# Optimization experiments

Hardware: AMD Instinct MI355X
Metric: run time of the kernel (lower is better)

The kernel has to match this reference:

```python
import jax, jax.numpy as jnp
import numpy as np

B = 8
A = 1614
TOPN = 6
IOU_THR = 0.25
PAD = 224
OUT = 224

def _make_anchors():
    # 6 anchor shapes on the 14x14 map, 6 on 7x7, 9 on 4x4 -> 1614 total,
    # ordered anchor-type-major then row-major spatial to match the [C,H,W] flatten
    # of the tidy conv outputs (as generate_default_anchor_maps does in NTS-Net).
    specs = [
        (14, 32.0, [(48, 48), (64, 48), (48, 64), (80, 80), (96, 64), (64, 96)]),
        (7, 64.0, [(96, 96), (128, 96), (96, 128), (160, 160), (192, 128), (128, 192)]),
        (4, 112.0, [(192, 192), (256, 192), (192, 256), (288, 288), (320, 256), (256, 320), (352, 352), (384, 320), (320, 384)]),
    ]
    blocks = []
    for fm, stride, sizes in specs:
        c = (np.arange(fm) + 0.5) * stride
        cy, cx = np.meshgrid(c, c, indexing='ij')
        for (h, w) in sizes:
            blocks.append(np.stack([cy - h / 2, cx - w / 2, cy + h / 2, cx + w / 2], -1).reshape(-1, 4))
    a = (np.concatenate(blocks, 0) + PAD).astype(np.int64)  # mimic (edge_anchors+224).astype(int)
    return a.astype(np.float32)  # [1614,4] (y0,x0,y1,x1) in padded-image coords

def _conv(x, w, b, stride, pad):
    y = jax.lax.conv_general_dilated(x, w, (stride, stride), [(pad, pad), (pad, pad)],
                                     dimension_numbers=('NCHW', 'OIHW', 'NCHW'))
    return y + b[None, :, None, None]

def _rpn_scores(rpn, wd1, bd1, wd2, bd2, wd3, bd3, wt1, bt1, wt2, bt2, wt3, bt3):
    b = rpn.shape[0]
    d1 = jax.nn.relu(_conv(rpn, wd1, bd1, 1, 1))   # [B,128,14,14]
    d2 = jax.nn.relu(_conv(d1, wd2, bd2, 2, 1))    # [B,128,7,7]
    d3 = jax.nn.relu(_conv(d2, wd3, bd3, 2, 1))    # [B,128,4,4]
    t1 = _conv(d1, wt1, bt1, 1, 0).reshape(b, -1)  # [B,1176]
    t2 = _conv(d2, wt2, bt2, 1, 0).reshape(b, -1)  # [B,294]
    t3 = _conv(d3, wt3, bt3, 1, 0).reshape(b, -1)  # [B,144]
    return jnp.concatenate([t1, t2, t3], axis=1)   # [B,1614]

def _nms_keep(boxes, scores):
    # Greedy NMS over all A anchors; returns keep mask in ORIGINAL anchor order.
    order = jnp.argsort(-scores)
    b = boxes[order]
    y0, x0, y1, x1 = b[:, 0], b[:, 1], b[:, 2], b[:, 3]
    area = (y1 - y0) * (x1 - x0)
    ih = jnp.clip(jnp.minimum(y1[:, None], y1[None, :]) - jnp.maximum(y0[:, None], y0[None, :]), 0)
    iw = jnp.clip(jnp.minimum(x1[:, None], x1[None, :]) - jnp.maximum(x0[:, None], x0[None, :]), 0)
    inter = ih * iw
    iou = inter / (area[:, None] + area[None, :] - inter)
    idx = jnp.arange(A)
    def body(i, supp):
        row = (iou[i] > IOU_THR) & (idx > i)
        return jnp.where(supp[i], supp, supp | row)
    supp = jax.lax.fori_loop(0, A, body, jnp.zeros((A,), bool))
    return jnp.zeros((A,), bool).at[order].set(~supp)

def _crop_resize(img, box):
    # img [3,Hp,Wp]; box int32 (x0,y0,x1,y1).
    # Equivalent to F.interpolate(img[:, y0:y1, x0:x1], (224,224), 'bilinear', align_corners=True)
    x0, y0, x1, y1 = box[0], box[1], box[2], box[3]
    t = jnp.arange(OUT, dtype=jnp.float32) / (OUT - 1)
    sy = y0.astype(jnp.float32) + t * (y1 - 1 - y0).astype(jnp.float32)
    sx = x0.astype(jnp.float32) + t * (x1 - 1 - x0).astype(jnp.float32)
    y0i = jnp.floor(sy).astype(jnp.int32); x0i = jnp.floor(sx).astype(jnp.int32)
    y1i = jnp.minimum(y0i + 1, y1 - 1);    x1i = jnp.minimum(x0i + 1, x1 - 1)
    wy = (sy - y0i.astype(jnp.float32))[None, :, None]
    wx = (sx - x0i.astype(jnp.float32))[None, None, :]
    g = lambda yi, xi: img[:, yi][:, :, xi]  # gather rows then cols -> [3,224,224]
    top = (1 - wx) * g(y0i, x0i) + wx * g(y0i, x1i)
    bot = (1 - wx) * g(y1i, x0i) + wx * g(y1i, x1i)
    return (1 - wy) * top + wy * bot

def setup_inputs():
    key = jax.random.key(0)
    ks = jax.random.split(key, 16)
    n = jax.random.normal
    return {
        'x': n(ks[0], (B, 3, 448, 448), jnp.float32),
        'rpn_feature': n(ks[1], (B, 2048, 14, 14), jnp.float32),
        'anchors': jnp.asarray(_make_anchors()),
        'wd1': 0.02 * n(ks[2], (128, 2048, 3, 3), jnp.float32), 'bd1': 0.01 * n(ks[3], (128,), jnp.float32),
        'wd2': 0.05 * n(ks[4], (128, 128, 3, 3), jnp.float32),  'bd2': 0.01 * n(ks[5], (128,), jnp.float32),
        'wd3': 0.05 * n(ks[6], (128, 128, 3, 3), jnp.float32),  'bd3': 0.01 * n(ks[7], (128,), jnp.float32),
        'wt1': 0.1 * n(ks[8], (6, 128, 1, 1), jnp.float32),     'bt1': 0.01 * n(ks[9], (6,), jnp.float32),
        'wt2': 0.1 * n(ks[10], (6, 128, 1, 1), jnp.float32),    'bt2': 0.01 * n(ks[11], (6,), jnp.float32),
        'wt3': 0.1 * n(ks[12], (9, 128, 1, 1), jnp.float32),    'bt3': 0.01 * n(ks[13], (9,), jnp.float32),
    }

def reference(x, rpn_feature, anchors, wd1, bd1, wd2, bd2, wd3, bd3, wt1, bt1, wt2, bt2, wt3, bt3):
    scores = _rpn_scores(rpn_feature, wd1, bd1, wd2, bd2, wd3, bd3, wt1, bt1, wt2, bt2, wt3, bt3)
    keep = jax.vmap(lambda s: _nms_keep(anchors, s))(scores)           # [B,A] bool
    masked = jnp.where(keep, scores, -jnp.inf)
    top_prob, top_idx = jax.lax.top_k(masked, TOPN)                    # [B,6]
    tb = anchors[top_idx]                                              # [B,6,4] (y0,x0,y1,x1)
    coords = jnp.stack([tb[..., 1], tb[..., 0], tb[..., 3], tb[..., 2]], -1)  # (x0,y0,x1,y1)
    x_pad = jnp.pad(x, ((0, 0), (0, 0), (PAD, PAD), (PAD, PAD)))       # [B,3,896,896]
    bint = coords.astype(jnp.int32)
    part_imgs = jax.vmap(lambda img, bs: jax.vmap(lambda bb: _crop_resize(img, bb))(bs))(x_pad, bint)  # [B,6,3,224,224]
    return part_imgs, coords, top_prob, top_idx
```

## Files before the change

### kernel.cpp

```cpp
#include <hip/hip_runtime.h>
#include <hip/hip_bf16.h>
#include <math.h>
#include <stdint.h>


#define OFF_COORDS 7225344
#define OFF_PROB   7225536
#define OFF_IDX    7225584
#define NA 1614
#define K1TOT 18432

typedef __attribute__((ext_vector_type(8)))  short  short8;
typedef __attribute__((ext_vector_type(16))) float  floatx16;

__device__ inline void split_bf16(float v, unsigned short& h, unsigned short& l)
{
    __hip_bfloat16 hb = __float2bfloat16(v);
    float hv = __bfloat162float(hb);
    __hip_bfloat16 lb = __float2bfloat16(v - hv);
    h = *reinterpret_cast<unsigned short*>(&hb);
    l = *reinterpret_cast<unsigned short*>(&lb);
}

__global__ __launch_bounds__(256) void k_prep(const float* __restrict__ rpn,
                                              const float* __restrict__ w1,
                                              const float* __restrict__ w2,
                                              const float* __restrict__ w3,
                                              unsigned short* __restrict__ ah,
                                              unsigned short* __restrict__ al,
                                              unsigned short* __restrict__ b1h,
                                              unsigned short* __restrict__ b1l,
                                              unsigned short* __restrict__ b2h,
                                              unsigned short* __restrict__ b2l,
                                              unsigned short* __restrict__ b3h,
                                              unsigned short* __restrict__ b3l)
{
    __shared__ float tileA[64][65];
    __shared__ float tileB[9][260];
    const int bid = blockIdx.x;
    const int t   = threadIdx.x;

    if (bid < 1024) {
        const int cib  = (bid & 31) * 64;
        const int posb = ((bid >> 5) & 3) * 64;
        const int b    = bid >> 7;
#pragma unroll
        for (int it = 0; it < 16; ++it) {
            int idx  = it * 256 + t;
            int cil  = idx >> 6;
            int posl = idx & 63;
            int pos  = posb + posl;
            int py = pos >> 4, px = pos & 15;
            int y = py - 1, x = px - 1;
            float v = 0.0f;
            if ((unsigned)y < 14u && (unsigned)x < 14u)
                v = rpn[((size_t)(b * 2048 + cib + cil) * 14 + y) * 14 + x];
            tileA[cil][posl] = v;
        }
        __syncthreads();
#pragma unroll
        for (int it = 0; it < 16; ++it) {
            int idx  = it * 256 + t;
            int posl = idx >> 6;
            int cil  = idx & 63;
            float v = tileA[cil][posl];
            unsigned short h, l;
            split_bf16(v, h, l);
            size_t o = (size_t)(b * 256 + posb + posl) * 2048 + cib + cil;
            ah[o] = h; al[o] = l;
        }
    } else if (bid < 2048) {
        const int lb  = bid - 1024;
        const int ci0 = (lb & 7) * 256;
        const int co  = lb >> 3;
        const float* wc = w1 + (size_t)co * K1TOT + (size_t)ci0 * 9;
#pragma unroll
        for (int it = 0; it < 9; ++it) {
            int i = it * 256 + t;
            float v = wc[i];
            tileB[i % 9][i / 9] = v;
        }
        __syncthreads();
#pragma unroll
        for (int tap = 0; tap < 9; ++tap) {
            float v = tileB[tap][t];
            unsigned short h, l;
            split_bf16(v, h, l);
            size_t o = (size_t)co * K1TOT + (size_t)tap * 2048 + ci0 + t;
            b1h[o] = h; b1l[o] = l;
        }
    } else {
        const int lb  = bid - 2048;
        const int tap = lb % 9;
        const int co  = lb / 9;
        const int z   = t >> 7;
        const int ci  = t & 127;
        const float* w = z ? w3 : w2;
        unsigned short* bh = z ? b3h : b2h;
        unsigned short* bl = z ? b3l : b2l;
        float v = w[((size_t)co * 128 + ci) * 9 + tap];
        unsigned short h, l;
        split_bf16(v, h, l);
        size_t o = (size_t)co * 1152 + tap * 128 + ci;
        bh[o] = h; bl[o] = l;
    }
}

template<int POSN, int OW, int STR, int CIN, int MTOT>
__global__ __launch_bounds__(128) void k_conv64(const short* __restrict__ ah,
                                                const short* __restrict__ al,
                                                const short* __restrict__ bh,
                                                const short* __restrict__ bl,
                                                float* __restrict__ partial,
                                                int chunk)
{
    constexpr int KTOT = CIN * 9;
    __shared__ short AsH[64][40];
    __shared__ short AsL[64][40];
    __shared__ short BsH[128][40];
    __shared__ short BsL[128][40];

    const int t     = threadIdx.x;
    const int lane  = t & 63;
    const int w     = t >> 6;
    const int wn    = w * 64;
    const int lm    = lane & 31;
    const int half  = lane >> 5;
    const int mbase = blockIdx.x * 64;
    const int kc    = blockIdx.y;
    const int k0    = kc * chunk;
    const int k1    = (k0 + chunk < KTOT) ? (k0 + chunk) : KTOT;

    const int akc = (t & 3) * 8;
    int arow[2], apos[2]; bool aval[2];
#pragma unroll
    for (int i = 0; i < 2; ++i) {
        int slot = i * 128 + t;
        int row  = slot >> 2;
        int m    = mbase + row;
        arow[i] = row;
        aval[i] = (m < MTOT);
        int mm = aval[i] ? m : 0;
        int b  = mm / POSN;
        int p  = mm - b * POSN;
        int y  = p / OW;
        int x  = p - y * OW;
        apos[i] = b * 256 + y * STR * 16 + x * STR;
    }

    floatx16 acc[2][2];
#pragma unroll
    for (int mf = 0; mf < 2; ++mf)
#pragma unroll
        for (int nf = 0; nf < 2; ++nf)
#pragma unroll
            for (int r = 0; r < 16; ++r) acc[mf][nf][r] = 0.0f;

    const short8 zero8 = {0, 0, 0, 0, 0, 0, 0, 0};

    for (int ks = k0; ks < k1; ks += 32) {
        const int tap = ks / CIN;
        const int ci0 = ks - tap * CIN;
        const int dy  = tap / 3, dx = tap - dy * 3;
#pragma unroll
        for (int i = 0; i < 2; ++i) {
            short8 vh = zero8, vl = zero8;
            if (aval[i]) {
                size_t g = (size_t)(apos[i] + dy * 16 + dx) * CIN + ci0 + akc;
                vh = *(const short8*)(ah + g);
                vl = *(const short8*)(al + g);
            }
            *(short8*)&AsH[arow[i]][akc] = vh;
            *(short8*)&AsL[arow[i]][akc] = vl;
        }
#pragma unroll
        for (int j = 0; j < 4; ++j) {
            int n = ((j * 128 + t) >> 2);
            size_t g = (size_t)n * KTOT + ks + akc;
            *(short8*)&BsH[n][akc] = *(const short8*)(bh + g);
            *(short8*)&BsL[n][akc] = *(const short8*)(bl + g);
        }
        __syncthreads();
#pragma unroll
        for (int kst = 0; kst < 2; ++kst) {
            const int koff = kst * 16 + half * 8;
            short8 a_h[2], a_l[2], b_h[2], b_l[2];
#pragma unroll
            for (int mf = 0; mf < 2; ++mf) {
                a_h[mf] = *(const short8*)&AsH[mf * 32 + lm][koff];
                a_l[mf] = *(const short8*)&AsL[mf * 32 + lm][koff];
            }
#pragma unroll
            for (int nf = 0; nf < 2; ++nf) {
                b_h[nf] = *(const short8*)&BsH[wn + nf * 32 + lm][koff];
                b_l[nf] = *(const short8*)&BsL[wn + nf * 32 + lm][koff];
            }
#pragma unroll
            for (int mf = 0; mf < 2; ++mf)
#pragma unroll
                for (int nf = 0; nf < 2; ++nf) {
                    acc[mf][nf] = __builtin_amdgcn_mfma_f32_32x32x16_bf16(
                        a_h[mf], b_h[nf], acc[mf][nf], 0, 0, 0);
                    acc[mf][nf] = __builtin_amdgcn_mfma_f32_32x32x16_bf16(
                        a_h[mf], b_l[nf], acc[mf][nf], 0, 0, 0);
                    acc[mf][nf] = __builtin_amdgcn_mfma_f32_32x32x16_bf16(
                        a_l[mf], b_h[nf], acc[mf][nf], 0, 0, 0);
                }
        }
        __syncthreads();
    }

    float* P = partial + (size_t)kc * MTOT * 128;
#pragma unroll
    for (int mf = 0; mf < 2; ++mf)
#pragma unroll
        for (int nf = 0; nf < 2; ++nf)
#pragma unroll
            for (int r = 0; r < 16; ++r) {
                int row = (r & 3) + 8 * (r >> 2) + 4 * half;
                int m = mbase + mf * 32 + row;
                int n = wn + nf * 32 + lm;
                if (m < MTOT) P[(size_t)m * 128 + n] = acc[mf][nf][r];
            }
}

template<int POSN, int OWV>
__global__ __launch_bounds__(256) void k_reduce_pad(const float* __restrict__ partial,
                                                    const float* __restrict__ bias,
                                                    float* __restrict__ dn,
                                                    __hip_bfloat16* __restrict__ ph,
                                                    __hip_bfloat16* __restrict__ pl,
                                                    int S)
{
    constexpr int MTOT = 8 * POSN;
    int idx = blockIdx.x * 256 + threadIdx.x;
    int b   = idx >> 13;
    int pos = (idx >> 5) & 255;
    int c4  = idx & 31;
    int y = (pos >> 4) - 1;
    int x = (pos & 15) - 1;
    if ((unsigned)y < (unsigned)OWV && (unsigned)x < (unsigned)OWV) {
        int m = b * POSN + y * OWV + x;
        float4 s = ((const float4*)bias)[c4];
        for (int k = 0; k < S; ++k) {
            float4 p = ((const float4*)(partial + (size_t)k * MTOT * 128 + (size_t)m * 128))[c4];
            s.x += p.x; s.y += p.y; s.z += p.z; s.w += p.w;
        }
        s.x = fmaxf(s.x, 0.0f); s.y = fmaxf(s.y, 0.0f);
        s.z = fmaxf(s.z, 0.0f); s.w = fmaxf(s.w, 0.0f);
        ((float4*)dn)[(size_t)m * 32 + c4] = s;
        ushort4 h, l;
        split_bf16(s.x, h.x, l.x);
        split_bf16(s.y, h.y, l.y);
        split_bf16(s.z, h.z, l.z);
        split_bf16(s.w, h.w, l.w);
        ((ushort4*)ph)[idx] = h;
        ((ushort4*)pl)[idx] = l;
    } else {
        ushort4 z = {0, 0, 0, 0};
        ((ushort4*)ph)[idx] = z;
        ((ushort4*)pl)[idx] = z;
    }
}

__global__ __launch_bounds__(256) void k_reduce3(const float* __restrict__ partial,
                                                 const float* __restrict__ bias,
                                                 float* __restrict__ dn, int S)
{
    int idx = blockIdx.x * 256 + threadIdx.x;
    int c4  = idx & 31;
    float4 s = ((const float4*)bias)[c4];
    for (int k = 0; k < S; ++k) {
        float4 p = ((const float4*)(partial + (size_t)k * 128 * 128))[idx];
        s.x += p.x; s.y += p.y; s.z += p.z; s.w += p.w;
    }
    s.x = fmaxf(s.x, 0.0f); s.y = fmaxf(s.y, 0.0f);
    s.z = fmaxf(s.z, 0.0f); s.w = fmaxf(s.w, 0.0f);
    ((float4*)dn)[idx] = s;
}

__global__ __launch_bounds__(512) void k_headnms(const float* __restrict__ d1n,
                                                 const float* __restrict__ d2n,
                                                 const float* __restrict__ d3n,
                                                 const float* __restrict__ w1, const float* __restrict__ b1,
                                                 const float* __restrict__ w2, const float* __restrict__ b2,
                                                 const float* __restrict__ w3, const float* __restrict__ b3,
                                                 const float* __restrict__ anchors,
                                                 float* __restrict__ out,
                                                 int* __restrict__ boxes)
{
    __shared__ float ms[NA];
    __shared__ float ay0[NA], ax0[NA], ay1[NA], ax1[NA];
    __shared__ unsigned char picked[NA];
    __shared__ float wsm[21 * 128];
    __shared__ float bsm[21];
    __shared__ float rv[8]; __shared__ int ri[8];
    __shared__ float win[5];
    const int b = blockIdx.x;
    const int t = threadIdx.x;

    for (int i = t; i < 21 * 128; i += 512)
        wsm[i] = (i < 768) ? w1[i] : (i < 1536) ? w2[i - 768] : w3[i - 1536];
    if (t < 21) bsm[t] = (t < 6) ? b1[t] : (t < 12) ? b2[t - 6] : b3[t - 12];
    for (int i = t; i < NA; i += 512) {
        float4 an = ((const float4*)anchors)[i];
        ay0[i] = an.x; ax0[i] = an.y; ay1[i] = an.z; ax1[i] = an.w;
        picked[i] = 0;
    }
    __syncthreads();

    for (int e = t; e < NA; e += 512) {
        const float* d; int wrow;
        if (e < 1176) {
            int c = e / 196, p = e - c * 196;
            d = d1n + (size_t)(b * 196 + p) * 128; wrow = c;
        } else if (e < 1470) {
            int e2 = e - 1176; int c = e2 / 49, p = e2 - c * 49;
            d = d2n + (size_t)(b * 49 + p) * 128; wrow = 6 + c;
        } else {
            int e2 = e - 1470; int c = e2 / 16, p = e2 - c * 16;
            d = d3n + (size_t)(b * 16 + p) * 128; wrow = 12 + c;
        }
        float s = bsm[wrow];
        const float4* wv4 = (const float4*)&wsm[wrow * 128];
#pragma unroll
        for (int i = 0; i < 32; ++i) {
            float4 dv = ((const float4*)d)[i];
            float4 wv = wv4[i];
            s = fmaf(dv.x, wv.x, s);
            s = fmaf(dv.y, wv.y, s);
            s = fmaf(dv.z, wv.z, s);
            s = fmaf(dv.w, wv.w, s);
        }
        ms[e] = s;
    }
    __syncthreads();

    for (int r = 0; r < 6; ++r) {
        float bv = -INFINITY; int bi = NA;
        for (int i = t; i < NA; i += 512) {
            if (!picked[i]) {
                float v = ms[i];
                if (v > bv || (v == bv && i < bi)) { bv = v; bi = i; }
            }
        }
#pragma unroll
        for (int off = 32; off > 0; off >>= 1) {
            float v2 = __shfl_down(bv, off);
            int   i2 = __shfl_down(bi, off);
            if (v2 > bv || (v2 == bv && i2 < bi)) { bv = v2; bi = i2; }
        }
        if ((t & 63) == 0) { rv[t >> 6] = bv; ri[t >> 6] = bi; }
        __syncthreads();
        if (t == 0) {
            bv = rv[0]; bi = ri[0];
            for (int wv = 1; wv < 8; ++wv)
                if (rv[wv] > bv || (rv[wv] == bv && ri[wv] < bi)) { bv = rv[wv]; bi = ri[wv]; }
            picked[bi] = 1;
            win[0] = ay0[bi]; win[1] = ax0[bi]; win[2] = ay1[bi]; win[3] = ax1[bi]; win[4] = bv;
            int o = b * 6 + r;
            out[OFF_COORDS + o * 4 + 0] = ax0[bi];
            out[OFF_COORDS + o * 4 + 1] = ay0[bi];
            out[OFF_COORDS + o * 4 + 2] = ax1[bi];
            out[OFF_COORDS + o * 4 + 3] = ay1[bi];
            out[OFF_PROB + o] = bv;
            out[OFF_IDX  + o] = (float)bi;
            boxes[o * 4 + 0] = (int)ax0[bi];
            boxes[o * 4 + 1] = (int)ay0[bi];
            boxes[o * 4 + 2] = (int)ax1[bi];
            boxes[o * 4 + 3] = (int)ay1[bi];
        }
        __syncthreads();
        float by0 = win[0], bx0 = win[1], by1 = win[2], bx1 = win[3];
        float barea = (by1 - by0) * (bx1 - bx0);
        for (int i = t; i < NA; i += 512) {
            if (picked[i]) continue;
            float ih = fmaxf(fminf(by1, ay1[i]) - fmaxf(by0, ay0[i]), 0.0f);
            float iw = fmaxf(fminf(bx1, ax1[i]) - fmaxf(bx0, ax0[i]), 0.0f);
            float inter = ih * iw;
            float area  = (ay1[i] - ay0[i]) * (ax1[i] - ax0[i]);
            float iou = inter / (barea + area - inter);
            if (iou > 0.25f) ms[i] = -INFINITY;
        }
        __syncthreads();
    }
}

__global__ __launch_bounds__(256) void k_crop(const float* __restrict__ x,
                                              const int* __restrict__ boxes,
                                              float* __restrict__ out)
{
    int idx = blockIdx.x * 256 + threadIdx.x;
    int i   = idx % 224;
    int j   = (idx / 224) % 224;
    int rem = idx / 50176;
    int c   = rem % 3;
    int br  = rem / 3;
    int b   = br / 6;
    int4 bx = ((const int4*)boxes)[br];
    float tj = (float)j / 223.0f;
    float sy = (float)bx.y + tj * (float)(bx.w - 1 - bx.y);
    int y0i = (int)floorf(sy);
    int y1i = min(y0i + 1, bx.w - 1);
    float wy = sy - (float)y0i;
    float ti = (float)i / 223.0f;
    float sx = (float)bx.x + ti * (float)(bx.z - 1 - bx.x);
    int x0i = (int)floorf(sx);
    int x1i = min(x0i + 1, bx.z - 1);
    float wx = sx - (float)x0i;
    const float* img = x + ((size_t)b * 3 + c) * 448 * 448;
    auto g = [&](int yy, int xx) -> float {
        yy -= 224; xx -= 224;
        if ((unsigned)yy >= 448u || (unsigned)xx >= 448u) return 0.0f;
        return img[(size_t)yy * 448 + xx];
    };
    float g00 = g(y0i, x0i), g01 = g(y0i, x1i);
    float g10 = g(y1i, x0i), g11 = g(y1i, x1i);
    float top = (1.0f - wx) * g00 + wx * g01;
    float bot = (1.0f - wx) * g10 + wx * g11;
    out[idx] = (1.0f - wy) * top + wy * bot;
}

extern "C" void kernel_launch(void* const* d_in, const int* in_sizes, int n_in,
                              void* d_out, int out_size, void* d_ws, size_t ws_size,
                              hipStream_t stream)
{
    (void)in_sizes; (void)n_in; (void)out_size;
    const float* x    = (const float*)d_in[0];
    const float* rpn  = (const float*)d_in[1];
    const float* anch = (const float*)d_in[2];
    const float* wd1  = (const float*)d_in[3];
    const float* bd1  = (const float*)d_in[4];
    const float* wd2  = (const float*)d_in[5];
    const float* bd2  = (const float*)d_in[6];
    const float* wd3  = (const float*)d_in[7];
    const float* bd3  = (const float*)d_in[8];
    const float* hw1  = (const float*)d_in[9];
    const float* hb1  = (const float*)d_in[10];
    const float* hw2  = (const float*)d_in[11];
    const float* hb2  = (const float*)d_in[12];
    const float* hw3  = (const float*)d_in[13];
    const float* hb3  = (const float*)d_in[14];
    float* out = (float*)d_out;

    char* ws = (char*)d_ws;
    size_t off = 0;
    auto alloc = [&](size_t bytes) -> void* {
        void* p = ws + off;
        off = (off + bytes + 255) & ~(size_t)255;
        return p;
    };
    unsigned short* ahb = (unsigned short*)alloc((size_t)8 * 256 * 2048 * 2);
    unsigned short* alb = (unsigned short*)alloc((size_t)8 * 256 * 2048 * 2);
    unsigned short* b1h = (unsigned short*)alloc((size_t)128 * K1TOT * 2);
    unsigned short* b1l = (unsigned short*)alloc((size_t)128 * K1TOT * 2);
    unsigned short* b2h = (unsigned short*)alloc((size_t)128 * 1152 * 2);
    unsigned short* b2l = (unsigned short*)alloc((size_t)128 * 1152 * 2);
    unsigned short* b3h = (unsigned short*)alloc((size_t)128 * 1152 * 2);
    unsigned short* b3l = (unsigned short*)alloc((size_t)128 * 1152 * 2);
    __hip_bfloat16* d1ph = (__hip_bfloat16*)alloc((size_t)8 * 256 * 128 * 2);
    __hip_bfloat16* d1pl = (__hip_bfloat16*)alloc((size_t)8 * 256 * 128 * 2);
    __hip_bfloat16* d2ph = (__hip_bfloat16*)alloc((size_t)8 * 256 * 128 * 2);
    __hip_bfloat16* d2pl = (__hip_bfloat16*)alloc((size_t)8 * 256 * 128 * 2);
    float* d1n  = (float*)alloc((size_t)8 * 196 * 128 * 4);
    float* d2n  = (float*)alloc((size_t)8 * 49 * 128 * 4);
    float* d3n  = (float*)alloc((size_t)8 * 16 * 128 * 4);
    int*  boxes = (int*)alloc((size_t)8 * 6 * 4 * 4);
    size_t avail = (ws_size > off) ? (ws_size - off) : 0;
    float* P = (float*)(ws + off);

    long long s1 = (long long)(avail / ((size_t)1568 * 128 * 4));
    if (s1 > 48) s1 = 48;
    if (s1 < 1)  s1 = 1;
    int S1 = (int)s1;
    int chunk1 = ((K1TOT + S1 * 32 - 1) / (S1 * 32)) * 32;

    long long s2 = (long long)(avail / ((size_t)392 * 128 * 4));
    if (s2 > 36) s2 = 36;
    if (s2 < 1)  s2 = 1;
    int S2 = (int)s2;
    int chunk2 = ((1152 + S2 * 32 - 1) / (S2 * 32)) * 32;

    long long s3 = (long long)(avail / ((size_t)128 * 128 * 4));
    if (s3 > 36) s3 = 36;
    if (s3 < 1)  s3 = 1;
    int S3 = (int)s3;
    int chunk3 = ((1152 + S3 * 32 - 1) / (S3 * 32)) * 32;

    k_prep<<<dim3(3200), 256, 0, stream>>>(rpn, wd1, wd2, wd3,
        ahb, alb, b1h, b1l, b2h, b2l, b3h, b3l);

    k_conv64<196, 14, 1, 2048, 1568><<<dim3(25, S1), 128, 0, stream>>>(
        (const short*)ahb, (const short*)alb, (const short*)b1h, (const short*)b1l, P, chunk1);
    k_reduce_pad<196, 14><<<dim3(256), 256, 0, stream>>>(P, bd1, d1n, d1ph, d1pl, S1);

    k_conv64<49, 7, 2, 128, 392><<<dim3(7, S2), 128, 0, stream>>>(
        (const short*)d1ph, (const short*)d1pl, (const short*)b2h, (const short*)b2l, P, chunk2);
    k_reduce_pad<49, 7><<<dim3(256), 256, 0, stream>>>(P, bd2, d2n, d2ph, d2pl, S2);

    k_conv64<16, 4, 2, 128, 128><<<dim3(2, S3), 128, 0, stream>>>(
        (const short*)d2ph, (const short*)d2pl, (const short*)b3h, (const short*)b3l, P, chunk3);
    k_reduce3<<<dim3(16), 256, 0, stream>>>(P, bd3, d3n, S3);

    k_headnms<<<dim3(8), 512, 0, stream>>>(d1n, d2n, d3n,
        hw1, hb1, hw2, hb2, hw3, hb3, anch, out, boxes);

    k_crop<<<dim3(28224), 256, 0, stream>>>(x, boxes, out);
}
```

Measured before the change: 276.6 us.

## Use 128x128 MFMA conv tile, split head scoring from NMS, vectorize crop

Adds a 256-thread conv kernel with a 128x128 output tile (2x2 waves, 2x2 MFMA fragments) for the large first conv. This raises reuse of each loaded B tile and halves the number of M blocks. The head 1x1 convs move out of the 8-block NMS kernel into a grid-wide kernel, so only the NMS/top-k runs per batch. The crop now writes four outputs per thread as a float4. The split-K counts for conv2 and conv3 are hardcoded to 36, which assumes the workspace is large enough.

```diff
diff --git a/kernel.cpp b/kernel.cpp
--- a/kernel.cpp
+++ b/kernel.cpp
@@ -107,6 +107,123 @@
 }
 
 template<int POSN, int OW, int STR, int CIN, int MTOT>
+__global__ __launch_bounds__(256) void k_conv_mfma(const short* __restrict__ ah,
+                                                   const short* __restrict__ al,
+                                                   const short* __restrict__ bh,
+                                                   const short* __restrict__ bl,
+                                                   float* __restrict__ partial,
+                                                   int chunk)
+{
+    constexpr int KTOT = CIN * 9;
+    __shared__ short AsH[128][40];
+    __shared__ short AsL[128][40];
+    __shared__ short BsH[128][40];
+    __shared__ short BsL[128][40];
+
+    const int t     = threadIdx.x;
+    const int lane  = t & 63;
+    const int w     = t >> 6;
+    const int wm    = (w & 1) * 64;
+    const int wn    = (w >> 1) * 64;
+    const int lm    = lane & 31;
+    const int half  = lane >> 5;
+    const int mbase = blockIdx.x * 128;
+    const int k0    = blockIdx.y * chunk;
+    const int k1    = (k0 + chunk < KTOT) ? (k0 + chunk) : KTOT;
+
+    int arow[2], apos[2]; bool aval[2];
+    const int akc = (t & 3) * 8;
+#pragma unroll
+    for (int i = 0; i < 2; ++i) {
+        int row = ((i * 256 + t) >> 2);
+        int m   = mbase + row;
+        arow[i] = row;
+        aval[i] = (m < MTOT);
+        int mm = aval[i] ? m : 0;
+        int b  = mm / POSN;
+        int p  = mm - b * POSN;
+        int y  = p / OW;
+        int x  = p - y * OW;
+        apos[i] = b * 256 + y * STR * 16 + x * STR;
+    }
+
+    floatx16 acc[2][2];
+#pragma unroll
+    for (int mf = 0; mf < 2; ++mf)
+#pragma unroll
+        for (int nf = 0; nf < 2; ++nf)
+#pragma unroll
+            for (int r = 0; r < 16; ++r) acc[mf][nf][r] = 0.0f;
+
+    const short8 zero8 = {0, 0, 0, 0, 0, 0, 0, 0};
+
+    for (int ks = k0; ks < k1; ks += 32) {
+        const int tap = ks / CIN;
+        const int ci0 = ks - tap * CIN;
+        const int dy  = tap / 3, dx = tap - dy * 3;
+#pragma unroll
+        for (int i = 0; i < 2; ++i) {
+            short8 vh = zero8, vl = zero8;
+            if (aval[i]) {
+                size_t g = (size_t)(apos[i] + dy * 16 + dx) * CIN + ci0 + akc;
+                vh = *(const short8*)(ah + g);
+                vl = *(const short8*)(al + g);
+            }
+            *(short8*)&AsH[arow[i]][akc] = vh;
+            *(short8*)&AsL[arow[i]][akc] = vl;
+        }
+#pragma unroll
+        for (int i = 0; i < 2; ++i) {
+            int n = ((i * 256 + t) >> 2);
+            size_t g = (size_t)n * KTOT + ks + akc;
+            *(short8*)&BsH[n][akc] = *(const short8*)(bh + g);
+            *(short8*)&BsL[n][akc] = *(const short8*)(bl + g);
+        }
+        __syncthreads();
+#pragma unroll
+        for (int kst = 0; kst < 2; ++kst) {
+            const int koff = kst * 16 + half * 8;
+            short8 a_h[2], a_l[2], b_h[2], b_l[2];
+#pragma unroll
+            for (int mf = 0; mf < 2; ++mf) {
+                a_h[mf] = *(const short8*)&AsH[wm + mf * 32 + lm][koff];
+                a_l[mf] = *(const short8*)&AsL[wm + mf * 32 + lm][koff];
+            }
+#pragma unroll
+            for (int nf = 0; nf < 2; ++nf) {
+                b_h[nf] = *(const short8*)&BsH[wn + nf * 32 + lm][koff];
+                b_l[nf] = *(const short8*)&BsL[wn + nf * 32 + lm][koff];
+            }
+#pragma unroll
+            for (int mf = 0; mf < 2; ++mf)
+#pragma unroll
+                for (int nf = 0; nf < 2; ++nf) {
+                    acc[mf][nf] = __builtin_amdgcn_mfma_f32_32x32x16_bf16(
+                        a_h[mf], b_h[nf], acc[mf][nf], 0, 0, 0);
+                    acc[mf][nf] = __builtin_amdgcn_mfma_f32_32x32x16_bf16(
+                        a_h[mf], b_l[nf], acc[mf][nf], 0, 0, 0);
+                    acc[mf][nf] = __builtin_amdgcn_mfma_f32_32x32x16_bf16(
+                        a_l[mf], b_h[nf], acc[mf][nf], 0, 0, 0);
+                }
+        }
+        __syncthreads();
+    }
+
+    float* P = partial + (size_t)blockIdx.y * MTOT * 128;
+#pragma unroll
+    for (int mf = 0; mf < 2; ++mf)
+#pragma unroll
+        for (int nf = 0; nf < 2; ++nf)
+#pragma unroll
+            for (int r = 0; r < 16; ++r) {
+                int row = (r & 3) + 8 * (r >> 2) + 4 * half;
+                int m = mbase + wm + mf * 32 + row;
+                int n = wn + nf * 32 + lm;
+                if (m < MTOT) P[(size_t)m * 128 + n] = acc[mf][nf][r];
+            }
+}
+
+template<int POSN, int OW, int STR, int CIN, int MTOT>
 __global__ __launch_bounds__(128) void k_conv64(const short* __restrict__ ah,
                                                 const short* __restrict__ al,
                                                 const short* __restrict__ bh,
@@ -279,66 +396,64 @@
     ((float4*)dn)[idx] = s;
 }
 
-__global__ __launch_bounds__(512) void k_headnms(const float* __restrict__ d1n,
-                                                 const float* __restrict__ d2n,
-                                                 const float* __restrict__ d3n,
-                                                 const float* __restrict__ w1, const float* __restrict__ b1,
-                                                 const float* __restrict__ w2, const float* __restrict__ b2,
-                                                 const float* __restrict__ w3, const float* __restrict__ b3,
-                                                 const float* __restrict__ anchors,
-                                                 float* __restrict__ out,
-                                                 int* __restrict__ boxes)
+__global__ __launch_bounds__(256) void k_heads(const float* __restrict__ d1n,
+                                               const float* __restrict__ d2n,
+                                               const float* __restrict__ d3n,
+                                               const float* __restrict__ w1, const float* __restrict__ b1,
+                                               const float* __restrict__ w2, const float* __restrict__ b2,
+                                               const float* __restrict__ w3, const float* __restrict__ b3,
+                                               float* __restrict__ scores)
+{
+    int idx = blockIdx.x * 256 + threadIdx.x;
+    if (idx >= 8 * NA) return;
+    int b = idx / NA;
+    int e = idx - b * NA;
+    const float* d; const float* w; float bias;
+    if (e < 1176) {
+        int c = e / 196, p = e - c * 196;
+        d = d1n + (size_t)(b * 196 + p) * 128; w = w1 + c * 128; bias = b1[c];
+    } else if (e < 1470) {
+        int e2 = e - 1176; int c = e2 / 49, p = e2 - c * 49;
+        d = d2n + (size_t)(b * 49 + p) * 128; w = w2 + c * 128; bias = b2[c];
+    } else {
+        int e2 = e - 1470; int c = e2 / 16, p = e2 - c * 16;
+        d = d3n + (size_t)(b * 16 + p) * 128; w = w3 + c * 128; bias = b3[c];
+    }
+    float s = bias;
+#pragma unroll
+    for (int i = 0; i < 32; ++i) {
+        float4 dv = ((const float4*)d)[i];
+        float4 wv = ((const float4*)w)[i];
+        s = fmaf(dv.x, wv.x, s);
+        s = fmaf(dv.y, wv.y, s);
+        s = fmaf(dv.z, wv.z, s);
+        s = fmaf(dv.w, wv.w, s);
+    }
+    scores[idx] = s;
+}
+
+__global__ __launch_bounds__(256) void k_nms_topk(const float* __restrict__ scores,
+                                                  const float* __restrict__ anchors,
+                                                  float* __restrict__ out,
+                                                  int* __restrict__ boxes)
 {
     __shared__ float ms[NA];
     __shared__ float ay0[NA], ax0[NA], ay1[NA], ax1[NA];
     __shared__ unsigned char picked[NA];
-    __shared__ float wsm[21 * 128];
-    __shared__ float bsm[21];
-    __shared__ float rv[8]; __shared__ int ri[8];
+    __shared__ float rv[4]; __shared__ int ri[4];
     __shared__ float win[5];
-    const int b = blockIdx.x;
-    const int t = threadIdx.x;
-
-    for (int i = t; i < 21 * 128; i += 512)
-        wsm[i] = (i < 768) ? w1[i] : (i < 1536) ? w2[i - 768] : w3[i - 1536];
-    if (t < 21) bsm[t] = (t < 6) ? b1[t] : (t < 12) ? b2[t - 6] : b3[t - 12];
-    for (int i = t; i < NA; i += 512) {
+    int b = blockIdx.x;
+    int t = threadIdx.x;
+    for (int i = t; i < NA; i += 256) {
+        ms[i] = scores[b * NA + i];
         float4 an = ((const float4*)anchors)[i];
         ay0[i] = an.x; ax0[i] = an.y; ay1[i] = an.z; ax1[i] = an.w;
         picked[i] = 0;
     }
     __syncthreads();
-
-    for (int e = t; e < NA; e += 512) {
-        const float* d; int wrow;
-        if (e < 1176) {
-            int c = e / 196, p = e - c * 196;
-            d = d1n + (size_t)(b * 196 + p) * 128; wrow = c;
-        } else if (e < 1470) {
-            int e2 = e - 1176; int c = e2 / 49, p = e2 - c * 49;
-            d = d2n + (size_t)(b * 49 + p) * 128; wrow = 6 + c;
-        } else {
-            int e2 = e - 1470; int c = e2 / 16, p = e2 - c * 16;
-            d = d3n + (size_t)(b * 16 + p) * 128; wrow = 12 + c;
-        }
-        float s = bsm[wrow];
-        const float4* wv4 = (const float4*)&wsm[wrow * 128];
-#pragma unroll
-        for (int i = 0; i < 32; ++i) {
-            float4 dv = ((const float4*)d)[i];
-            float4 wv = wv4[i];
-            s = fmaf(dv.x, wv.x, s);
-            s = fmaf(dv.y, wv.y, s);
-            s = fmaf(dv.z, wv.z, s);
-            s = fmaf(dv.w, wv.w, s);
-        }
-        ms[e] = s;
-    }
-    __syncthreads();
-
     for (int r = 0; r < 6; ++r) {
         float bv = -INFINITY; int bi = NA;
-        for (int i = t; i < NA; i += 512) {
+        for (int i = t; i < NA; i += 256) {
             if (!picked[i]) {
                 float v = ms[i];
                 if (v > bv || (v == bv && i < bi)) { bv = v; bi = i; }
@@ -354,7 +469,7 @@
         __syncthreads();
         if (t == 0) {
             bv = rv[0]; bi = ri[0];
-            for (int wv = 1; wv < 8; ++wv)
+            for (int wv = 1; wv < 4; ++wv)
                 if (rv[wv] > bv || (rv[wv] == bv && ri[wv] < bi)) { bv = rv[wv]; bi = ri[wv]; }
             picked[bi] = 1;
             win[0] = ay0[bi]; win[1] = ax0[bi]; win[2] = ay1[bi]; win[3] = ax1[bi]; win[4] = bv;
@@ -373,7 +488,7 @@
         __syncthreads();
         float by0 = win[0], bx0 = win[1], by1 = win[2], bx1 = win[3];
         float barea = (by1 - by0) * (bx1 - bx0);
-        for (int i = t; i < NA; i += 512) {
+        for (int i = t; i < NA; i += 256) {
             if (picked[i]) continue;
             float ih = fmaxf(fminf(by1, ay1[i]) - fmaxf(by0, ay0[i]), 0.0f);
             float iw = fmaxf(fminf(bx1, ax1[i]) - fmaxf(bx0, ax0[i]), 0.0f);
@@ -386,14 +501,14 @@
     }
 }
 
-__global__ __launch_bounds__(256) void k_crop(const float* __restrict__ x,
-                                              const int* __restrict__ boxes,
-                                              float* __restrict__ out)
+__global__ __launch_bounds__(256) void k_crop4(const float* __restrict__ x,
+                                               const int* __restrict__ boxes,
+                                               float* __restrict__ out)
 {
     int idx = blockIdx.x * 256 + threadIdx.x;
-    int i   = idx % 224;
-    int j   = (idx / 224) % 224;
-    int rem = idx / 50176;
+    int qi  = idx % 56;
+    int j   = (idx / 56) % 224;
+    int rem = idx / (56 * 224);
     int c   = rem % 3;
     int br  = rem / 3;
     int b   = br / 6;
@@ -403,22 +518,30 @@
     int y0i = (int)floorf(sy);
     int y1i = min(y0i + 1, bx.w - 1);
     float wy = sy - (float)y0i;
-    float ti = (float)i / 223.0f;
-    float sx = (float)bx.x + ti * (float)(bx.z - 1 - bx.x);
-    int x0i = (int)floorf(sx);
-    int x1i = min(x0i + 1, bx.z - 1);
-    float wx = sx - (float)x0i;
     const float* img = x + ((size_t)b * 3 + c) * 448 * 448;
     auto g = [&](int yy, int xx) -> float {
         yy -= 224; xx -= 224;
         if ((unsigned)yy >= 448u || (unsigned)xx >= 448u) return 0.0f;
         return img[(size_t)yy * 448 + xx];
     };
-    float g00 = g(y0i, x0i), g01 = g(y0i, x1i);
-    float g10 = g(y1i, x0i), g11 = g(y1i, x1i);
-    float top = (1.0f - wx) * g00 + wx * g01;
-    float bot = (1.0f - wx) * g10 + wx * g11;
-    out[idx] = (1.0f - wy) * top + wy * bot;
+    float4 o;
+#pragma unroll
+    for (int e = 0; e < 4; ++e) {
+        int i = qi * 4 + e;
+        float ti = (float)i / 223.0f;
+        float sx = (float)bx.x + ti * (float)(bx.z - 1 - bx.x);
+        int x0i = (int)floorf(sx);
+        int x1i = min(x0i + 1, bx.z - 1);
+        float wx = sx - (float)x0i;
+        float g00 = g(y0i, x0i), g01 = g(y0i, x1i);
+        float g10 = g(y1i, x0i), g11 = g(y1i, x1i);
+        float top = (1.0f - wx) * g00 + wx * g01;
+        float bot = (1.0f - wx) * g10 + wx * g11;
+        float v = (1.0f - wy) * top + wy * bot;
+        if (e == 0) o.x = v; else if (e == 1) o.y = v;
+        else if (e == 2) o.z = v; else o.w = v;
+    }
+    ((float4*)out)[idx] = o;
 }
 
 extern "C" void kernel_launch(void* const* d_in, const int* in_sizes, int n_in,
@@ -465,6 +588,7 @@
     float* d1n  = (float*)alloc((size_t)8 * 196 * 128 * 4);
     float* d2n  = (float*)alloc((size_t)8 * 49 * 128 * 4);
     float* d3n  = (float*)alloc((size_t)8 * 16 * 128 * 4);
+    float* sc   = (float*)alloc((size_t)8 * NA * 4);
     int*  boxes = (int*)alloc((size_t)8 * 6 * 4 * 4);
     size_t avail = (ws_size > off) ? (ws_size - off) : 0;
     float* P = (float*)(ws + off);
@@ -475,35 +599,25 @@
     int S1 = (int)s1;
     int chunk1 = ((K1TOT + S1 * 32 - 1) / (S1 * 32)) * 32;
 
-    long long s2 = (long long)(avail / ((size_t)392 * 128 * 4));
-    if (s2 > 36) s2 = 36;
-    if (s2 < 1)  s2 = 1;
-    int S2 = (int)s2;
-    int chunk2 = ((1152 + S2 * 32 - 1) / (S2 * 32)) * 32;
-
-    long long s3 = (long long)(avail / ((size_t)128 * 128 * 4));
-    if (s3 > 36) s3 = 36;
-    if (s3 < 1)  s3 = 1;
-    int S3 = (int)s3;
-    int chunk3 = ((1152 + S3 * 32 - 1) / (S3 * 32)) * 32;
-
     k_prep<<<dim3(3200), 256, 0, stream>>>(rpn, wd1, wd2, wd3,
         ahb, alb, b1h, b1l, b2h, b2l, b3h, b3l);
 
-    k_conv64<196, 14, 1, 2048, 1568><<<dim3(25, S1), 128, 0, stream>>>(
+    k_conv_mfma<196, 14, 1, 2048, 1568><<<dim3(13, S1), 256, 0, stream>>>(
         (const short*)ahb, (const short*)alb, (const short*)b1h, (const short*)b1l, P, chunk1);
     k_reduce_pad<196, 14><<<dim3(256), 256, 0, stream>>>(P, bd1, d1n, d1ph, d1pl, S1);
 
-    k_conv64<49, 7, 2, 128, 392><<<dim3(7, S2), 128, 0, stream>>>(
-        (const short*)d1ph, (const short*)d1pl, (const short*)b2h, (const short*)b2l, P, chunk2);
-    k_reduce_pad<49, 7><<<dim3(256), 256, 0, stream>>>(P, bd2, d2n, d2ph, d2pl, S2);
-
-    k_conv64<16, 4, 2, 128, 128><<<dim3(2, S3), 128, 0, stream>>>(
-        (const short*)d2ph, (const short*)d2pl, (const short*)b3h, (const short*)b3l, P, chunk3);
-    k_reduce3<<<dim3(16), 256, 0, stream>>>(P, bd3, d3n, S3);
-
-    k_headnms<<<dim3(8), 512, 0, stream>>>(d1n, d2n, d3n,
-        hw1, hb1, hw2, hb2, hw3, hb3, anch, out, boxes);
-
-    k_crop<<<dim3(28224), 256, 0, stream>>>(x, boxes, out);
-}
+    k_conv64<49, 7, 2, 128, 392><<<dim3(7, 36), 128, 0, stream>>>(
+        (const short*)d1ph, (const short*)d1pl, (const short*)b2h, (const short*)b2l, P, 32);
+    k_reduce_pad<49, 7><<<dim3(256), 256, 0, stream>>>(P, bd2, d2n, d2ph, d2pl, 36);
+
+    k_conv64<16, 4, 2, 128, 128><<<dim3(2, 36), 128, 0, stream>>>(
+        (const short*)d2ph, (const short*)d2pl, (const short*)b3h, (const short*)b3l, P, 32);
+    k_reduce3<<<dim3(16), 256, 0, stream>>>(P, bd3, d3n, 36);
+
+    k_heads<<<dim3((8 * NA + 255) / 256), 256, 0, stream>>>(d1n, d2n, d3n,
+        hw1, hb1, hw2, hb2, hw3, hb3, sc);
+
+    k_nms_topk<<<dim3(8), 256, 0, stream>>>(sc, anch, out, boxes);
+
+    k_crop4<<<dim3(7056), 256, 0, stream>>>(x, boxes, out);
+}
```

After: 253.7 us. 8.3% less time.
